# Kernel optimization log

Measured on AMD Instinct MI355X. Metric: run time of the kernel, lower is better.

The kernel has to match this reference:

```python
import jax, jax.numpy as jnp
import numpy as np

D_MODEL = 1024
N_HEADS = 16
N_KV_HEADS = 4
HEAD_DIM = D_MODEL // N_HEADS  # 64
N_REP = N_HEADS // N_KV_HEADS  # 4
THETA = 10000.0
LOGIT_CAP = 30.0
EPS = 1e-6
SCALE = HEAD_DIM ** -0.5


def rmsnorm(x, w):
    return x * jax.lax.rsqrt(jnp.mean(x * x, axis=-1, keepdims=True) + EPS) * w


def rope_tables(seq_len, dtype):
    inv_freq = 1.0 / (THETA ** (jnp.arange(0, HEAD_DIM, 2, dtype=jnp.float32) / HEAD_DIM))
    t = jnp.arange(seq_len, dtype=jnp.float32)
    freqs = jnp.outer(t, inv_freq)                      # [S, hd/2]
    emb = jnp.concatenate([freqs, freqs], axis=-1)      # [S, hd]
    return jnp.cos(emb).astype(dtype), jnp.sin(emb).astype(dtype)


def rotate_half(x):
    x1, x2 = jnp.split(x, 2, axis=-1)
    return jnp.concatenate([-x2, x1], axis=-1)


def apply_rope(x, cos, sin):
    # x: [B, H, S, hd]; cos/sin: [S, hd] broadcast over (B, H)
    return x * cos + rotate_half(x) * sin


def setup_inputs() -> dict:
    key = jax.random.key(0)
    ks = jax.random.split(key, 7)
    B, S = 4, 2048
    w = 0.02
    return {
        "x": jax.random.normal(ks[0], (B, S, D_MODEL), dtype=jnp.float32),
        "Wq": jax.random.normal(ks[1], (N_HEADS * HEAD_DIM, D_MODEL), dtype=jnp.float32) * w,
        "Wk": jax.random.normal(ks[2], (N_KV_HEADS * HEAD_DIM, D_MODEL), dtype=jnp.float32) * w,
        "Wv": jax.random.normal(ks[3], (N_KV_HEADS * HEAD_DIM, D_MODEL), dtype=jnp.float32) * w,
        "Wo": jax.random.normal(ks[4], (D_MODEL, N_HEADS * HEAD_DIM), dtype=jnp.float32) * w,
        "q_norm_w": jnp.ones((HEAD_DIM,), dtype=jnp.float32),
        "k_norm_w": jnp.ones((HEAD_DIM,), dtype=jnp.float32),
    }


def reference(x, Wq, Wk, Wv, Wo, q_norm_w, k_norm_w):
    B, S, _ = x.shape
    # projections (nn.Linear: y = x @ W^T)
    q = (x @ Wq.T).reshape(B, S, N_HEADS, HEAD_DIM).transpose(0, 2, 1, 3)      # [B,H,S,d]
    k = (x @ Wk.T).reshape(B, S, N_KV_HEADS, HEAD_DIM).transpose(0, 2, 1, 3)   # [B,Hkv,S,d]
    v = (x @ Wv.T).reshape(B, S, N_KV_HEADS, HEAD_DIM).transpose(0, 2, 1, 3)
    # QK-RMSNorm
    q = rmsnorm(q, q_norm_w)
    k = rmsnorm(k, k_norm_w)
    # RoPE
    cos, sin = rope_tables(S, x.dtype)
    q = apply_rope(q, cos, sin)
    k = apply_rope(k, cos, sin)
    # GQA expand (repeat_interleave over head dim)
    k_exp = jnp.repeat(k, N_REP, axis=1)  # [B,H,S,d]
    v_exp = jnp.repeat(v, N_REP, axis=1)
    # soft-capped attention (training path)
    scores = jnp.einsum('bhqd,bhkd->bhqk', q, k_exp) * SCALE
    scores = LOGIT_CAP * jnp.tanh(scores / LOGIT_CAP)
    causal = jnp.triu(jnp.ones((S, S), dtype=bool), k=1)  # kv_len - seq_len + 1 = 1
    scores = jnp.where(causal, -jnp.inf, scores)
    attn = jax.nn.softmax(scores, axis=-1)
    out = jnp.einsum('bhqk,bhkd->bhqd', attn, v_exp)
    out = out.transpose(0, 2, 1, 3).reshape(B, S, N_HEADS * HEAD_DIM)
    return out @ Wo.T
```

## Files before the change

kernel.cpp:

```cpp
#include <hip/hip_runtime.h>
#include <hip/hip_bf16.h>
#include <math.h>
#include <stdint.h>

#define D_MODEL 1024
#define NHEADS  16
#define NKV     4
#define HD      64
#define SEQ     2048
#define BATCH   4
#define MTOK    (BATCH*SEQ)
#define NQKV    (D_MODEL + 2*NKV*HD)
#define ASCALE  0.125f
#define CAP     30.0f

using f32x4  = __attribute__((ext_vector_type(4))) float;
using f32x2  = __attribute__((ext_vector_type(2))) float;
using bf16x8 = __attribute__((ext_vector_type(8))) short;
using u32x4  = __attribute__((ext_vector_type(4))) unsigned int;

__device__ __forceinline__ unsigned short f2bf(float f) {
  union { float f; unsigned u; } v; v.f = f;
  unsigned u = v.u + 0x7fffu + ((v.u >> 16) & 1u);
  return (unsigned short)(u >> 16);
}
__device__ __forceinline__ unsigned short f2bf_hup(float f) {
  union { float f; unsigned u; } v; v.f = f;
  return (unsigned short)((v.u + 0x8000u) >> 16);
}
__device__ __forceinline__ float fexp2(float x) {
  return __builtin_amdgcn_exp2f(x);
}
__device__ __forceinline__ void async_copy16(void* lds, const void* g) {
  __builtin_amdgcn_global_load_lds(
      (const __attribute__((address_space(1))) unsigned int*)(uintptr_t)g,
      (__attribute__((address_space(3))) unsigned int*)(uintptr_t)lds, 16, 0, 0);
}

__global__ __launch_bounds__(256) void cvt_all(
    const float* __restrict__ x, const float* __restrict__ wq,
    const float* __restrict__ wk, const float* __restrict__ wv,
    const float* __restrict__ wo,
    unsigned short* __restrict__ xb, unsigned short* __restrict__ wqkv,
    unsigned short* __restrict__ wob) {
  const long i = (long)(blockIdx.x * 256 + threadIdx.x) * 4;
  const float* src; unsigned short* dst; long off;
  if (i < 8388608L)      { src = x;  dst = xb;             off = i; }
  else if (i < 9437184L) { src = wq; dst = wqkv;           off = i - 8388608L; }
  else if (i < 9699328L) { src = wk; dst = wqkv + 1048576; off = i - 9437184L; }
  else if (i < 9961472L) { src = wv; dst = wqkv + 1310720; off = i - 9699328L; }
  else                   { src = wo; dst = wob;            off = i - 9961472L; }
  float4 v = *(const float4*)(src + off);
  ushort4 o; o.x = f2bf(v.x); o.y = f2bf(v.y); o.z = f2bf(v.z); o.w = f2bf(v.w);
  *(ushort4*)(dst + off) = o;
}

__global__ __launch_bounds__(256) void gemm_qkv(
    const unsigned short* __restrict__ A, const unsigned short* __restrict__ B,
    const float* __restrict__ qw, const float* __restrict__ kw,
    unsigned short* __restrict__ Qn, unsigned short* __restrict__ Kn,
    unsigned short* __restrict__ Vt) {
  __shared__ __align__(16) unsigned short As[2][128 * 32];
  __shared__ __align__(16) unsigned short Bs[2][128 * 32];
  const int t = threadIdx.x;
  const int w = t >> 6, l = t & 63;
  const int mb = blockIdx.x, nb = blockIdx.y;
  const int wm = w & 1, wn = w >> 1;
  const int quad = l >> 4, ln = l & 15;
  const int K = D_MODEL;
  f32x4 acc[4][4] = {};
  const unsigned short* Ag = A + (size_t)(mb * 128 + w * 32) * K;
  const unsigned short* Bg = B + (size_t)(nb * 128 + w * 32) * K;
  const int lrow = l >> 2, lcol = (l & 3) * 8;
  const int wo16 = w * 2048 + l * 16;

  async_copy16((char*)As[0] + wo16,        Ag + (size_t)lrow * K + lcol);
  async_copy16((char*)As[0] + wo16 + 1024, Ag + (size_t)(16 + lrow) * K + lcol);
  async_copy16((char*)Bs[0] + wo16,        Bg + (size_t)lrow * K + lcol);
  async_copy16((char*)Bs[0] + wo16 + 1024, Bg + (size_t)(16 + lrow) * K + lcol);

  int cur = 0;
  for (int kb = 0; kb < K; kb += 32) {
    __syncthreads();
    if (kb + 32 < K) {
      const int kn = kb + 32;
      async_copy16((char*)As[cur ^ 1] + wo16,        Ag + (size_t)lrow * K + kn + lcol);
      async_copy16((char*)As[cur ^ 1] + wo16 + 1024, Ag + (size_t)(16 + lrow) * K + kn + lcol);
      async_copy16((char*)Bs[cur ^ 1] + wo16,        Bg + (size_t)lrow * K + kn + lcol);
      async_copy16((char*)Bs[cur ^ 1] + wo16 + 1024, Bg + (size_t)(16 + lrow) * K + kn + lcol);
    }
    bf16x8 af[4], bfr[4];
#pragma unroll
    for (int mt = 0; mt < 4; ++mt)
      af[mt] = *(const bf16x8*)(As[cur] + (wm * 64 + mt * 16 + ln) * 32 + quad * 8);
#pragma unroll
    for (int nt = 0; nt < 4; ++nt)
      bfr[nt] = *(const bf16x8*)(Bs[cur] + (wn * 64 + nt * 16 + ln) * 32 + quad * 8);
#pragma unroll
    for (int mt = 0; mt < 4; ++mt)
#pragma unroll
      for (int nt = 0; nt < 4; ++nt)
        acc[mt][nt] = __builtin_amdgcn_mfma_f32_16x16x32_bf16(af[mt], bfr[nt], acc[mt][nt], 0, 0, 0);
    cur ^= 1;
  }

  const int hs = nb * 2 + wn;
  const int bB = mb >> 4;
  const int sBase = ((mb & 15) * 128) + wm * 64;

  if (hs < 20) {
    const float* wgt = (hs < 16) ? qw : kw;
    float wv_[4];
#pragma unroll
    for (int nt = 0; nt < 4; ++nt) wv_[nt] = wgt[nt * 16 + ln];
    const float f0 = __expf(-(float)ln * 0.2878231366f);
    const float f1 = f0 * 0.01f;
    unsigned short* dst = (hs < 16)
        ? Qn + (size_t)(bB * 16 + hs) * SEQ * 64
        : Kn + (size_t)(bB * 4 + (hs - 16)) * SEQ * 64;
#pragma unroll
    for (int mt = 0; mt < 4; ++mt) {
#pragma unroll
      for (int r = 0; r < 4; ++r) {
        const int sTok = sBase + mt * 16 + quad * 4 + r;
        float ss = 0.f;
#pragma unroll
        for (int nt = 0; nt < 4; ++nt) ss = fmaf(acc[mt][nt][r], acc[mt][nt][r], ss);
        ss += __shfl_xor(ss, 1, 64); ss += __shfl_xor(ss, 2, 64);
        ss += __shfl_xor(ss, 4, 64); ss += __shfl_xor(ss, 8, 64);
        const float inv = rsqrtf(ss * (1.0f / 64.0f) + 1e-6f);
        float xn[4];
#pragma unroll
        for (int nt = 0; nt < 4; ++nt) xn[nt] = acc[mt][nt][r] * inv * wv_[nt];
        float sn0, cs0, sn1, cs1;
        __sincosf((float)sTok * f0, &sn0, &cs0);
        __sincosf((float)sTok * f1, &sn1, &cs1);
        const float o0 = xn[0] * cs0 - xn[2] * sn0;
        const float o1 = xn[1] * cs1 - xn[3] * sn1;
        const float o2 = xn[2] * cs0 + xn[0] * sn0;
        const float o3 = xn[3] * cs1 + xn[1] * sn1;
        const size_t ro = (size_t)sTok * 64 + ln;
        dst[ro]      = f2bf(o0);
        dst[ro + 16] = f2bf(o1);
        dst[ro + 32] = f2bf(o2);
        dst[ro + 48] = f2bf(o3);
      }
    }
  } else {
    unsigned short* dst = Vt + (size_t)(bB * 4 + (hs - 20)) * 64 * SEQ;
#pragma unroll
    for (int mt = 0; mt < 4; ++mt)
#pragma unroll
      for (int nt = 0; nt < 4; ++nt)
#pragma unroll
        for (int r = 0; r < 4; ++r) {
          const int sTok = sBase + mt * 16 + quad * 4 + r;
          dst[(size_t)(nt * 16 + ln) * SEQ + sTok] = f2bf(acc[mt][nt][r]);
        }
  }
}

__global__ __launch_bounds__(256) void gemm_bt_f32(
    const unsigned short* __restrict__ A, const unsigned short* __restrict__ B,
    float* __restrict__ C, int M, int N, int K) {
  __shared__ __align__(16) unsigned short As[2][128 * 32];
  __shared__ __align__(16) unsigned short Bs[2][128 * 32];
  const int t = threadIdx.x;
  const int w = t >> 6, l = t & 63;
  const int mb = blockIdx.x, nb = blockIdx.y;
  const int wm = w & 1, wn = w >> 1;
  f32x4 acc[4][4] = {};
  const unsigned short* Ag = A + (size_t)(mb * 128 + w * 32) * K;
  const unsigned short* Bg = B + (size_t)(nb * 128 + w * 32) * K;
  const int lrow = l >> 2, lcol = (l & 3) * 8;
  const int wo16 = w * 2048 + l * 16;

  async_copy16((char*)As[0] + wo16,        Ag + (size_t)lrow * K + lcol);
  async_copy16((char*)As[0] + wo16 + 1024, Ag + (size_t)(16 + lrow) * K + lcol);
  async_copy16((char*)Bs[0] + wo16,        Bg + (size_t)lrow * K + lcol);
  async_copy16((char*)Bs[0] + wo16 + 1024, Bg + (size_t)(16 + lrow) * K + lcol);

  int cur = 0;
  for (int kb = 0; kb < K; kb += 32) {
    __syncthreads();
    if (kb + 32 < K) {
      const int kn = kb + 32;
      async_copy16((char*)As[cur ^ 1] + wo16,        Ag + (size_t)lrow * K + kn + lcol);
      async_copy16((char*)As[cur ^ 1] + wo16 + 1024, Ag + (size_t)(16 + lrow) * K + kn + lcol);
      async_copy16((char*)Bs[cur ^ 1] + wo16,        Bg + (size_t)lrow * K + kn + lcol);
      async_copy16((char*)Bs[cur ^ 1] + wo16 + 1024, Bg + (size_t)(16 + lrow) * K + kn + lcol);
    }
    bf16x8 af[4], bfr[4];
#pragma unroll
    for (int mt = 0; mt < 4; ++mt)
      af[mt] = *(const bf16x8*)(As[cur] + (wm * 64 + mt * 16 + (l & 15)) * 32 + (l >> 4) * 8);
#pragma unroll
    for (int nt = 0; nt < 4; ++nt)
      bfr[nt] = *(const bf16x8*)(Bs[cur] + (wn * 64 + nt * 16 + (l & 15)) * 32 + (l >> 4) * 8);
#pragma unroll
    for (int mt = 0; mt < 4; ++mt)
#pragma unroll
      for (int nt = 0; nt < 4; ++nt)
        acc[mt][nt] = __builtin_amdgcn_mfma_f32_16x16x32_bf16(af[mt], bfr[nt], acc[mt][nt], 0, 0, 0);
    cur ^= 1;
  }
  const int row0 = mb * 128 + wm * 64, col0 = nb * 128 + wn * 64;
#pragma unroll
  for (int mt = 0; mt < 4; ++mt)
#pragma unroll
    for (int nt = 0; nt < 4; ++nt)
#pragma unroll
      for (int r = 0; r < 4; ++r) {
        int row = row0 + mt * 16 + (l >> 4) * 4 + r;
        int col = col0 + nt * 16 + (l & 15);
        C[(size_t)row * N + col] = acc[mt][nt][r];
      }
}

__global__ __launch_bounds__(256, 4) void attn(
    const unsigned short* __restrict__ Qn, const unsigned short* __restrict__ Kn,
    const unsigned short* __restrict__ Vtg, unsigned short* __restrict__ O) {
  __shared__ __align__(16) unsigned short Ks[2][4096];
  __shared__ __align__(16) unsigned short Vs[2][4096];
  const int t = threadIdx.x, w = t >> 6, l = t & 63;
  const int quad = l >> 4, ln = l & 15;
  const int bid = blockIdx.x;
  const int qt = 15 - (bid >> 6);
  const int bh = bid & 63;
  const int h = bh & 15, b = bh >> 4;
  const int q0 = qt * 128;
  const int wq0 = q0 + w * 32;
  const unsigned short* Qh = Qn + ((size_t)(b * 16 + h)) * SEQ * 64;
  const unsigned short* Kg = Kn + ((size_t)(b * 4 + (h >> 2))) * SEQ * 64;
  const unsigned short* Vg = Vtg + ((size_t)(b * 4 + (h >> 2))) * 64 * SEQ;
  const int lrow = l >> 2;
  const int lswz = (((l & 3) ^ ((lrow >> 1) & 3)) * 8);
  const int qsw = (quad ^ ((ln >> 1) & 3)) << 4;

  bf16x8 aq[2][2];
#pragma unroll
  for (int mt = 0; mt < 2; ++mt)
#pragma unroll
    for (int ks = 0; ks < 2; ++ks)
      aq[mt][ks] = *(const bf16x8*)(Qh + (size_t)(wq0 + mt * 16 + ln) * 64 + ks * 32 + quad * 8);
  f32x4 o_acc[2][4] = {};
  f32x2 lp[2] = {};

  const float Cc = 0.18033688011112042f;
  const float B1 = -5.787037037e-6f;
  const float M2 = 11.541560327f;
  const int qr0 = wq0 + ln;

  const int jmax = 2 * qt + 2;

#pragma unroll
  for (int i = 0; i < 2; ++i) {
    int s = w * 2 + i;
    int snt = s >> 1, sks = s & 1;
    async_copy16((char*)Ks[0] + s * 1024,
                 Kg + (size_t)(snt * 16 + lrow) * 64 + sks * 32 + lswz);
    async_copy16((char*)Vs[0] + s * 1024,
                 Vg + (size_t)(snt * 16 + lrow) * SEQ + sks * 32 + lswz);
  }

  for (int jj = 0; jj < jmax; ++jj) {
    const int kv0 = jj * 64;
    const int cur = jj & 1;
    __syncthreads();
    if (jj + 1 < jmax) {
      const int kvn = kv0 + 64;
#pragma unroll
      for (int i = 0; i < 2; ++i) {
        int s = w * 2 + i;
        int snt = s >> 1, sks = s & 1;
        async_copy16((char*)Ks[cur ^ 1] + s * 1024,
                     Kg + (size_t)(kvn + snt * 16 + lrow) * 64 + sks * 32 + lswz);
        async_copy16((char*)Vs[cur ^ 1] + s * 1024,
                     Vg + (size_t)(snt * 16 + lrow) * SEQ + kvn + sks * 32 + lswz);
      }
    }
    if (kv0 > wq0 + 31) continue;

    f32x4 st[4][2] = {};
    __builtin_amdgcn_s_setprio(1);
#pragma unroll
    for (int nt = 0; nt < 4; ++nt)
#pragma unroll
      for (int ks = 0; ks < 2; ++ks) {
        bf16x8 bk = *(const bf16x8*)((char*)Ks[cur] + (nt * 2 + ks) * 1024 + ln * 64 + qsw);
        st[nt][0] = __builtin_amdgcn_mfma_f32_16x16x32_bf16(bk, aq[0][ks], st[nt][0], 0, 0, 0);
        st[nt][1] = __builtin_amdgcn_mfma_f32_16x16x32_bf16(bk, aq[1][ks], st[nt][1], 0, 0, 0);
      }
    __builtin_amdgcn_s_setprio(0);

    const bool needMask = (kv0 + 63 > wq0);
    bf16x8 ap[2][2];
#pragma unroll
    for (int mt = 0; mt < 2; ++mt) {
      const int qrow = qr0 + mt * 16;
      unsigned Wp[4][2];
#pragma unroll
      for (int nt = 0; nt < 4; ++nt)
#pragma unroll
        for (int rp = 0; rp < 2; ++rp) {
          f32x2 s = { st[nt][mt][rp * 2], st[nt][mt][rp * 2 + 1] };
          f32x2 s2 = s * s;
          f32x2 tt = s2 * B1 + 1.0f;
          f32x2 arg = (s * Cc) * tt - M2;
          float pr0 = fexp2(arg.x), pr1 = fexp2(arg.y);
          if (needMask) {
            const int kvb = kv0 + nt * 16 + quad * 4 + rp * 2;
            if (kvb > qrow)     pr0 = 0.0f;
            if (kvb + 1 > qrow) pr1 = 0.0f;
          }
          lp[mt] += (f32x2){pr0, pr1};
          unsigned wpk;
          asm("v_cvt_pk_bf16_f32 %0, %1, %2" : "=v"(wpk) : "v"(pr0), "v"(pr1));
          Wp[nt][rp] = wpk;
        }
#pragma unroll
      for (int ks = 0; ks < 2; ++ks) {
        unsigned a0 = Wp[2 * ks][0], b0 = Wp[2 * ks + 1][0];
        unsigned a1 = Wp[2 * ks][1], b1 = Wp[2 * ks + 1][1];
        asm("v_permlane32_swap_b32 %0, %1" : "+v"(a0), "+v"(b0));
        asm("v_permlane16_swap_b32 %0, %1" : "+v"(a0), "+v"(b0));
        asm("v_permlane32_swap_b32 %0, %1" : "+v"(a1), "+v"(b1));
        asm("v_permlane16_swap_b32 %0, %1" : "+v"(a1), "+v"(b1));
        union { u32x4 u; bf16x8 bv; } cc;
        cc.u = (u32x4){a0, a1, b0, b1};
        ap[mt][ks] = cc.bv;
      }
    }

    __builtin_amdgcn_s_setprio(1);
#pragma unroll
    for (int nt = 0; nt < 4; ++nt)
#pragma unroll
      for (int ks = 0; ks < 2; ++ks) {
        bf16x8 bv = *(const bf16x8*)((char*)Vs[cur] + (nt * 2 + ks) * 1024 + ln * 64 + qsw);
        o_acc[0][nt] = __builtin_amdgcn_mfma_f32_16x16x32_bf16(ap[0][ks], bv, o_acc[0][nt], 0, 0, 0);
        o_acc[1][nt] = __builtin_amdgcn_mfma_f32_16x16x32_bf16(ap[1][ks], bv, o_acc[1][nt], 0, 0, 0);
      }
    __builtin_amdgcn_s_setprio(0);
  }

  float invl[2][4];
#pragma unroll
  for (int mt = 0; mt < 2; ++mt) {
    float s = lp[mt].x + lp[mt].y;
    s += __shfl_xor(s, 16, 64);
    s += __shfl_xor(s, 32, 64);
#pragma unroll
    for (int r = 0; r < 4; ++r)
      invl[mt][r] = __builtin_amdgcn_rcpf(__shfl(s, quad * 4 + r, 64));
  }
#pragma unroll
  for (int mt = 0; mt < 2; ++mt)
#pragma unroll
    for (int nt = 0; nt < 4; ++nt)
#pragma unroll
      for (int r = 0; r < 4; ++r) {
        int qrow = wq0 + mt * 16 + quad * 4 + r;
        int col = h * 64 + nt * 16 + ln;
        O[((size_t)(b * SEQ + qrow)) * 1024 + col] = f2bf_hup(o_acc[mt][nt][r] * invl[mt][r]);
      }
}

extern "C" void kernel_launch(void* const* d_in, const int* in_sizes, int n_in,
                              void* d_out, int out_size, void* d_ws, size_t ws_size,
                              hipStream_t stream) {
  const float* x  = (const float*)d_in[0];
  const float* Wq = (const float*)d_in[1];
  const float* Wk = (const float*)d_in[2];
  const float* Wv = (const float*)d_in[3];
  const float* Wo = (const float*)d_in[4];
  const float* qw = (const float*)d_in[5];
  const float* kw = (const float*)d_in[6];
  float* out = (float*)d_out;

  char* ws = (char*)d_ws;
  unsigned short* xb   = (unsigned short*)(ws);
  unsigned short* wqkv = (unsigned short*)(ws + 16777216);
  unsigned short* wo   = (unsigned short*)(ws + 19922944);
  unsigned short* Qn   = (unsigned short*)(ws + 22020096);
  unsigned short* Kn   = (unsigned short*)(ws + 38797312);
  unsigned short* Vtg  = (unsigned short*)(ws + 42991616);
  unsigned short* Ob   = (unsigned short*)(ws + 47185920);

  cvt_all<<<10752, 256, 0, stream>>>(x, Wq, Wk, Wv, Wo, xb, wqkv, wo);
  gemm_qkv<<<dim3(MTOK / 128, NQKV / 128), 256, 0, stream>>>(xb, wqkv, qw, kw, Qn, Kn, Vtg);
  attn<<<1024, 256, 0, stream>>>(Qn, Kn, Vtg, Ob);
  gemm_bt_f32<<<dim3(MTOK / 128, 1024 / 128), 256, 0, stream>>>(Ob, wo, out, MTOK, 1024, 1024);
}
```

Baseline: 214.8 us.

## Enlarge projection GEMM tiles to 256x256 with 512-thread blocks

Both the fused QKV GEMM and the output projection GEMM now use 256x256 output tiles per block with 8 waves (2x4), each wave computing 128x64. This raises arithmetic intensity per LDS load and halves global reloads of A/B tiles. MFMA bursts are bracketed with s_setprio so that compute waves are favoured. The trade-off is fewer blocks (e.g. 32x6 and 32x4 grids on a 256-CU device), which risks underfilling the GPU, plus higher register pressure from 32 accumulators per lane.

```diff
diff --git a/kernel.cpp b/kernel.cpp
--- a/kernel.cpp
+++ b/kernel.cpp
@@ -55,58 +55,64 @@
   *(ushort4*)(dst + off) = o;
 }
 
-__global__ __launch_bounds__(256) void gemm_qkv(
+__global__ __launch_bounds__(512, 2) void gemm_qkv(
     const unsigned short* __restrict__ A, const unsigned short* __restrict__ B,
     const float* __restrict__ qw, const float* __restrict__ kw,
     unsigned short* __restrict__ Qn, unsigned short* __restrict__ Kn,
     unsigned short* __restrict__ Vt) {
-  __shared__ __align__(16) unsigned short As[2][128 * 32];
-  __shared__ __align__(16) unsigned short Bs[2][128 * 32];
+  __shared__ __align__(16) unsigned short LA[2][8192];
+  __shared__ __align__(16) unsigned short LB[2][8192];
   const int t = threadIdx.x;
   const int w = t >> 6, l = t & 63;
+  const int quad = l >> 4, ln = l & 15;
+  const int wm = w >> 2, wn = w & 3;
   const int mb = blockIdx.x, nb = blockIdx.y;
-  const int wm = w & 1, wn = w >> 1;
-  const int quad = l >> 4, ln = l & 15;
   const int K = D_MODEL;
-  f32x4 acc[4][4] = {};
-  const unsigned short* Ag = A + (size_t)(mb * 128 + w * 32) * K;
-  const unsigned short* Bg = B + (size_t)(nb * 128 + w * 32) * K;
-  const int lrow = l >> 2, lcol = (l & 3) * 8;
-  const int wo16 = w * 2048 + l * 16;
-
-  async_copy16((char*)As[0] + wo16,        Ag + (size_t)lrow * K + lcol);
-  async_copy16((char*)As[0] + wo16 + 1024, Ag + (size_t)(16 + lrow) * K + lcol);
-  async_copy16((char*)Bs[0] + wo16,        Bg + (size_t)lrow * K + lcol);
-  async_copy16((char*)Bs[0] + wo16 + 1024, Bg + (size_t)(16 + lrow) * K + lcol);
+  f32x4 acc[8][4] = {};
+  const unsigned short* Ag = A + (size_t)(mb * 256) * K;
+  const unsigned short* Bg = B + (size_t)(nb * 256) * K;
+  const int srow = t >> 2;
+  const int scol = (t & 3) * 8;
+  const int dst16 = t * 16;
+  const int abase = wm * 8192 + ln * 64 + quad * 16;
+  const int bbase = wn * 4096 + ln * 64 + quad * 16;
+
+  async_copy16((char*)LA[0] + dst16,        Ag + (size_t)srow * K + scol);
+  async_copy16((char*)LA[0] + dst16 + 8192, Ag + (size_t)(srow + 128) * K + scol);
+  async_copy16((char*)LB[0] + dst16,        Bg + (size_t)srow * K + scol);
+  async_copy16((char*)LB[0] + dst16 + 8192, Bg + (size_t)(srow + 128) * K + scol);
 
   int cur = 0;
   for (int kb = 0; kb < K; kb += 32) {
     __syncthreads();
     if (kb + 32 < K) {
       const int kn = kb + 32;
-      async_copy16((char*)As[cur ^ 1] + wo16,        Ag + (size_t)lrow * K + kn + lcol);
-      async_copy16((char*)As[cur ^ 1] + wo16 + 1024, Ag + (size_t)(16 + lrow) * K + kn + lcol);
-      async_copy16((char*)Bs[cur ^ 1] + wo16,        Bg + (size_t)lrow * K + kn + lcol);
-      async_copy16((char*)Bs[cur ^ 1] + wo16 + 1024, Bg + (size_t)(16 + lrow) * K + kn + lcol);
+      char* pa = (char*)LA[cur ^ 1]; char* pb = (char*)LB[cur ^ 1];
+      async_copy16(pa + dst16,        Ag + (size_t)srow * K + kn + scol);
+      async_copy16(pa + dst16 + 8192, Ag + (size_t)(srow + 128) * K + kn + scol);
+      async_copy16(pb + dst16,        Bg + (size_t)srow * K + kn + scol);
+      async_copy16(pb + dst16 + 8192, Bg + (size_t)(srow + 128) * K + kn + scol);
     }
-    bf16x8 af[4], bfr[4];
-#pragma unroll
-    for (int mt = 0; mt < 4; ++mt)
-      af[mt] = *(const bf16x8*)(As[cur] + (wm * 64 + mt * 16 + ln) * 32 + quad * 8);
-#pragma unroll
-    for (int nt = 0; nt < 4; ++nt)
-      bfr[nt] = *(const bf16x8*)(Bs[cur] + (wn * 64 + nt * 16 + ln) * 32 + quad * 8);
-#pragma unroll
-    for (int mt = 0; mt < 4; ++mt)
+    bf16x8 bf[4], af[8];
+#pragma unroll
+    for (int nt = 0; nt < 4; ++nt)
+      bf[nt] = *(const bf16x8*)((char*)LB[cur] + bbase + nt * 1024);
+#pragma unroll
+    for (int mt = 0; mt < 8; ++mt)
+      af[mt] = *(const bf16x8*)((char*)LA[cur] + abase + mt * 1024);
+    __builtin_amdgcn_s_setprio(1);
+#pragma unroll
+    for (int mt = 0; mt < 8; ++mt)
 #pragma unroll
       for (int nt = 0; nt < 4; ++nt)
-        acc[mt][nt] = __builtin_amdgcn_mfma_f32_16x16x32_bf16(af[mt], bfr[nt], acc[mt][nt], 0, 0, 0);
+        acc[mt][nt] = __builtin_amdgcn_mfma_f32_16x16x32_bf16(af[mt], bf[nt], acc[mt][nt], 0, 0, 0);
+    __builtin_amdgcn_s_setprio(0);
     cur ^= 1;
   }
 
-  const int hs = nb * 2 + wn;
-  const int bB = mb >> 4;
-  const int sBase = ((mb & 15) * 128) + wm * 64;
+  const int hs = nb * 4 + wn;
+  const int bB = mb >> 3;
+  const int sBase = ((mb & 7) * 256) + wm * 128;
 
   if (hs < 20) {
     const float* wgt = (hs < 16) ? qw : kw;
@@ -119,7 +125,7 @@
         ? Qn + (size_t)(bB * 16 + hs) * SEQ * 64
         : Kn + (size_t)(bB * 4 + (hs - 16)) * SEQ * 64;
 #pragma unroll
-    for (int mt = 0; mt < 4; ++mt) {
+    for (int mt = 0; mt < 8; ++mt) {
 #pragma unroll
       for (int r = 0; r < 4; ++r) {
         const int sTok = sBase + mt * 16 + quad * 4 + r;
@@ -149,7 +155,7 @@
   } else {
     unsigned short* dst = Vt + (size_t)(bB * 4 + (hs - 20)) * 64 * SEQ;
 #pragma unroll
-    for (int mt = 0; mt < 4; ++mt)
+    for (int mt = 0; mt < 8; ++mt)
 #pragma unroll
       for (int nt = 0; nt < 4; ++nt)
 #pragma unroll
@@ -160,59 +166,66 @@
   }
 }
 
-__global__ __launch_bounds__(256) void gemm_bt_f32(
+__global__ __launch_bounds__(512, 2) void gemm_bt_f32(
     const unsigned short* __restrict__ A, const unsigned short* __restrict__ B,
     float* __restrict__ C, int M, int N, int K) {
-  __shared__ __align__(16) unsigned short As[2][128 * 32];
-  __shared__ __align__(16) unsigned short Bs[2][128 * 32];
+  __shared__ __align__(16) unsigned short LA[2][8192];
+  __shared__ __align__(16) unsigned short LB[2][8192];
   const int t = threadIdx.x;
   const int w = t >> 6, l = t & 63;
+  const int quad = l >> 4, ln = l & 15;
+  const int wm = w >> 2, wn = w & 3;
   const int mb = blockIdx.x, nb = blockIdx.y;
-  const int wm = w & 1, wn = w >> 1;
-  f32x4 acc[4][4] = {};
-  const unsigned short* Ag = A + (size_t)(mb * 128 + w * 32) * K;
-  const unsigned short* Bg = B + (size_t)(nb * 128 + w * 32) * K;
-  const int lrow = l >> 2, lcol = (l & 3) * 8;
-  const int wo16 = w * 2048 + l * 16;
-
-  async_copy16((char*)As[0] + wo16,        Ag + (size_t)lrow * K + lcol);
-  async_copy16((char*)As[0] + wo16 + 1024, Ag + (size_t)(16 + lrow) * K + lcol);
-  async_copy16((char*)Bs[0] + wo16,        Bg + (size_t)lrow * K + lcol);
-  async_copy16((char*)Bs[0] + wo16 + 1024, Bg + (size_t)(16 + lrow) * K + lcol);
+  f32x4 acc[8][4] = {};
+  const unsigned short* Ag = A + (size_t)(mb * 256) * K;
+  const unsigned short* Bg = B + (size_t)(nb * 256) * K;
+  const int srow = t >> 2;
+  const int scol = (t & 3) * 8;
+  const int dst16 = t * 16;
+  const int abase = wm * 8192 + ln * 64 + quad * 16;
+  const int bbase = wn * 4096 + ln * 64 + quad * 16;
+
+  async_copy16((char*)LA[0] + dst16,        Ag + (size_t)srow * K + scol);
+  async_copy16((char*)LA[0] + dst16 + 8192, Ag + (size_t)(srow + 128) * K + scol);
+  async_copy16((char*)LB[0] + dst16,        Bg + (size_t)srow * K + scol);
+  async_copy16((char*)LB[0] + dst16 + 8192, Bg + (size_t)(srow + 128) * K + scol);
 
   int cur = 0;
   for (int kb = 0; kb < K; kb += 32) {
     __syncthreads();
     if (kb + 32 < K) {
       const int kn = kb + 32;
-      async_copy16((char*)As[cur ^ 1] + wo16,        Ag + (size_t)lrow * K + kn + lcol);
-      async_copy16((char*)As[cur ^ 1] + wo16 + 1024, Ag + (size_t)(16 + lrow) * K + kn + lcol);
-      async_copy16((char*)Bs[cur ^ 1] + wo16,        Bg + (size_t)lrow * K + kn + lcol);
-      async_copy16((char*)Bs[cur ^ 1] + wo16 + 1024, Bg + (size_t)(16 + lrow) * K + kn + lcol);
+      char* pa = (char*)LA[cur ^ 1]; char* pb = (char*)LB[cur ^ 1];
+      async_copy16(pa + dst16,        Ag + (size_t)srow * K + kn + scol);
+      async_copy16(pa + dst16 + 8192, Ag + (size_t)(srow + 128) * K + kn + scol);
+      async_copy16(pb + dst16,        Bg + (size_t)srow * K + kn + scol);
+      async_copy16(pb + dst16 + 8192, Bg + (size_t)(srow + 128) * K + kn + scol);
     }
-    bf16x8 af[4], bfr[4];
-#pragma unroll
-    for (int mt = 0; mt < 4; ++mt)
-      af[mt] = *(const bf16x8*)(As[cur] + (wm * 64 + mt * 16 + (l & 15)) * 32 + (l >> 4) * 8);
-#pragma unroll
-    for (int nt = 0; nt < 4; ++nt)
-      bfr[nt] = *(const bf16x8*)(Bs[cur] + (wn * 64 + nt * 16 + (l & 15)) * 32 + (l >> 4) * 8);
-#pragma unroll
-    for (int mt = 0; mt < 4; ++mt)
+    bf16x8 bf[4], af[8];
+#pragma unroll
+    for (int nt = 0; nt < 4; ++nt)
+      bf[nt] = *(const bf16x8*)((char*)LB[cur] + bbase + nt * 1024);
+#pragma unroll
+    for (int mt = 0; mt < 8; ++mt)
+      af[mt] = *(const bf16x8*)((char*)LA[cur] + abase + mt * 1024);
+    __builtin_amdgcn_s_setprio(1);
+#pragma unroll
+    for (int mt = 0; mt < 8; ++mt)
 #pragma unroll
       for (int nt = 0; nt < 4; ++nt)
-        acc[mt][nt] = __builtin_amdgcn_mfma_f32_16x16x32_bf16(af[mt], bfr[nt], acc[mt][nt], 0, 0, 0);
+        acc[mt][nt] = __builtin_amdgcn_mfma_f32_16x16x32_bf16(af[mt], bf[nt], acc[mt][nt], 0, 0, 0);
+    __builtin_amdgcn_s_setprio(0);
     cur ^= 1;
   }
-  const int row0 = mb * 128 + wm * 64, col0 = nb * 128 + wn * 64;
-#pragma unroll
-  for (int mt = 0; mt < 4; ++mt)
+  const int row0 = mb * 256 + wm * 128, col0 = nb * 256 + wn * 64;
+#pragma unroll
+  for (int mt = 0; mt < 8; ++mt)
 #pragma unroll
     for (int nt = 0; nt < 4; ++nt)
 #pragma unroll
       for (int r = 0; r < 4; ++r) {
-        int row = row0 + mt * 16 + (l >> 4) * 4 + r;
-        int col = col0 + nt * 16 + (l & 15);
+        int row = row0 + mt * 16 + quad * 4 + r;
+        int col = col0 + nt * 16 + ln;
         C[(size_t)row * N + col] = acc[mt][nt][r];
       }
 }
@@ -388,7 +401,7 @@
   unsigned short* Ob   = (unsigned short*)(ws + 47185920);
 
   cvt_all<<<10752, 256, 0, stream>>>(x, Wq, Wk, Wv, Wo, xb, wqkv, wo);
-  gemm_qkv<<<dim3(MTOK / 128, NQKV / 128), 256, 0, stream>>>(xb, wqkv, qw, kw, Qn, Kn, Vtg);
+  gemm_qkv<<<dim3(MTOK / 256, NQKV / 256), 512, 0, stream>>>(xb, wqkv, qw, kw, Qn, Kn, Vtg);
   attn<<<1024, 256, 0, stream>>>(Qn, Kn, Vtg, Ob);
-  gemm_bt_f32<<<dim3(MTOK / 128, 1024 / 128), 256, 0, stream>>>(Ob, wo, out, MTOK, 1024, 1024);
-}
+  gemm_bt_f32<<<dim3(MTOK / 256, 1024 / 256), 512, 0, stream>>>(Ob, wo, out, MTOK, 1024, 1024);
+}
```

New measurement: 229.0 us. +6.6%, slower.

## Fuse fp32-to-bf16 conversion of x into QKV GEMM A-tile loads

Applied to the files above, without the earlier changes.

The separate conversion pass over x is removed. The QKV GEMM now streams fp32 x tiles into a swizzled LDS buffer and converts them to bf16 with packed cvt instructions just before the MFMA. This saves a full read and write of the 32MB activation, at the cost of twice the LDS footprint and global traffic for the A tile, which is re-read once per N-block (12 times). It also folds one multiply out of the soft-cap polynomial in the attention inner loop by rescaling the coefficient.

```diff
diff --git a/kernel.cpp b/kernel.cpp
--- a/kernel.cpp
+++ b/kernel.cpp
@@ -37,30 +37,27 @@
       (__attribute__((address_space(3))) unsigned int*)(uintptr_t)lds, 16, 0, 0);
 }
 
-__global__ __launch_bounds__(256) void cvt_all(
-    const float* __restrict__ x, const float* __restrict__ wq,
-    const float* __restrict__ wk, const float* __restrict__ wv,
-    const float* __restrict__ wo,
-    unsigned short* __restrict__ xb, unsigned short* __restrict__ wqkv,
-    unsigned short* __restrict__ wob) {
+__global__ __launch_bounds__(256) void cvt_w(
+    const float* __restrict__ wq, const float* __restrict__ wk,
+    const float* __restrict__ wv, const float* __restrict__ wo,
+    unsigned short* __restrict__ wqkv, unsigned short* __restrict__ wob) {
   const long i = (long)(blockIdx.x * 256 + threadIdx.x) * 4;
   const float* src; unsigned short* dst; long off;
-  if (i < 8388608L)      { src = x;  dst = xb;             off = i; }
-  else if (i < 9437184L) { src = wq; dst = wqkv;           off = i - 8388608L; }
-  else if (i < 9699328L) { src = wk; dst = wqkv + 1048576; off = i - 9437184L; }
-  else if (i < 9961472L) { src = wv; dst = wqkv + 1310720; off = i - 9699328L; }
-  else                   { src = wo; dst = wob;            off = i - 9961472L; }
+  if (i < 1048576L)      { src = wq; dst = wqkv;           off = i; }
+  else if (i < 1310720L) { src = wk; dst = wqkv + 1048576; off = i - 1048576L; }
+  else if (i < 1572864L) { src = wv; dst = wqkv + 1310720; off = i - 1310720L; }
+  else                   { src = wo; dst = wob;            off = i - 1572864L; }
   float4 v = *(const float4*)(src + off);
   ushort4 o; o.x = f2bf(v.x); o.y = f2bf(v.y); o.z = f2bf(v.z); o.w = f2bf(v.w);
   *(ushort4*)(dst + off) = o;
 }
 
 __global__ __launch_bounds__(256) void gemm_qkv(
-    const unsigned short* __restrict__ A, const unsigned short* __restrict__ B,
+    const float* __restrict__ X, const unsigned short* __restrict__ B,
     const float* __restrict__ qw, const float* __restrict__ kw,
     unsigned short* __restrict__ Qn, unsigned short* __restrict__ Kn,
     unsigned short* __restrict__ Vt) {
-  __shared__ __align__(16) unsigned short As[2][128 * 32];
+  __shared__ __align__(16) float          Af[2][128 * 32];
   __shared__ __align__(16) unsigned short Bs[2][128 * 32];
   const int t = threadIdx.x;
   const int w = t >> 6, l = t & 63;
@@ -69,13 +66,22 @@
   const int quad = l >> 4, ln = l & 15;
   const int K = D_MODEL;
   f32x4 acc[4][4] = {};
-  const unsigned short* Ag = A + (size_t)(mb * 128 + w * 32) * K;
+  const float* Ag = X + (size_t)(mb * 128) * K;
   const unsigned short* Bg = B + (size_t)(nb * 128 + w * 32) * K;
   const int lrow = l >> 2, lcol = (l & 3) * 8;
   const int wo16 = w * 2048 + l * 16;
-
-  async_copy16((char*)As[0] + wo16,        Ag + (size_t)lrow * K + lcol);
-  async_copy16((char*)As[0] + wo16 + 1024, Ag + (size_t)(16 + lrow) * K + lcol);
+  int arow_[4], acol_[4];
+#pragma unroll
+  for (int i = 0; i < 4; ++i) {
+    const int s = t + i * 256;
+    arow_[i] = s >> 3;
+    acol_[i] = ((s & 7) ^ ((s >> 3) & 7)) * 4;
+  }
+
+#pragma unroll
+  for (int i = 0; i < 4; ++i)
+    async_copy16((char*)Af[0] + (t + i * 256) * 16,
+                 Ag + (size_t)arow_[i] * K + acol_[i]);
   async_copy16((char*)Bs[0] + wo16,        Bg + (size_t)lrow * K + lcol);
   async_copy16((char*)Bs[0] + wo16 + 1024, Bg + (size_t)(16 + lrow) * K + lcol);
 
@@ -84,15 +90,29 @@
     __syncthreads();
     if (kb + 32 < K) {
       const int kn = kb + 32;
-      async_copy16((char*)As[cur ^ 1] + wo16,        Ag + (size_t)lrow * K + kn + lcol);
-      async_copy16((char*)As[cur ^ 1] + wo16 + 1024, Ag + (size_t)(16 + lrow) * K + kn + lcol);
+#pragma unroll
+      for (int i = 0; i < 4; ++i)
+        async_copy16((char*)Af[cur ^ 1] + (t + i * 256) * 16,
+                     Ag + (size_t)arow_[i] * K + kn + acol_[i]);
       async_copy16((char*)Bs[cur ^ 1] + wo16,        Bg + (size_t)lrow * K + kn + lcol);
       async_copy16((char*)Bs[cur ^ 1] + wo16 + 1024, Bg + (size_t)(16 + lrow) * K + kn + lcol);
     }
     bf16x8 af[4], bfr[4];
 #pragma unroll
-    for (int mt = 0; mt < 4; ++mt)
-      af[mt] = *(const bf16x8*)(As[cur] + (wm * 64 + mt * 16 + ln) * 32 + quad * 8);
+    for (int mt = 0; mt < 4; ++mt) {
+      const int rr = wm * 64 + mt * 16 + ln;
+      const char* base = (const char*)Af[cur] + rr * 128;
+      const int sl0 = ((quad * 2)     ^ (rr & 7)) * 16;
+      const int sl1 = ((quad * 2 + 1) ^ (rr & 7)) * 16;
+      f32x4 v0 = *(const f32x4*)(base + sl0);
+      f32x4 v1 = *(const f32x4*)(base + sl1);
+      union { u32x4 u; bf16x8 b; } cv;
+      asm("v_cvt_pk_bf16_f32 %0, %1, %2" : "=v"(cv.u[0]) : "v"(v0.x), "v"(v0.y));
+      asm("v_cvt_pk_bf16_f32 %0, %1, %2" : "=v"(cv.u[1]) : "v"(v0.z), "v"(v0.w));
+      asm("v_cvt_pk_bf16_f32 %0, %1, %2" : "=v"(cv.u[2]) : "v"(v1.x), "v"(v1.y));
+      asm("v_cvt_pk_bf16_f32 %0, %1, %2" : "=v"(cv.u[3]) : "v"(v1.z), "v"(v1.w));
+      af[mt] = cv.b;
+    }
 #pragma unroll
     for (int nt = 0; nt < 4; ++nt)
       bfr[nt] = *(const bf16x8*)(Bs[cur] + (wn * 64 + nt * 16 + ln) * 32 + quad * 8);
@@ -246,9 +266,9 @@
   f32x4 o_acc[2][4] = {};
   f32x2 lp[2] = {};
 
-  const float Cc = 0.18033688011112042f;
-  const float B1 = -5.787037037e-6f;
-  const float M2 = 11.541560327f;
+  const float Cc  = 0.18033688011112042f;
+  const float B1c = -1.0436160e-6f;
+  const float M2  = 11.541560327f;
   const int qr0 = wq0 + ln;
 
   const int jmax = 2 * qt + 2;
@@ -305,8 +325,8 @@
         for (int rp = 0; rp < 2; ++rp) {
           f32x2 s = { st[nt][mt][rp * 2], st[nt][mt][rp * 2 + 1] };
           f32x2 s2 = s * s;
-          f32x2 tt = s2 * B1 + 1.0f;
-          f32x2 arg = (s * Cc) * tt - M2;
+          f32x2 tt = s2 * B1c + Cc;
+          f32x2 arg = s * tt - M2;
           float pr0 = fexp2(arg.x), pr1 = fexp2(arg.y);
           if (needMask) {
             const int kvb = kv0 + nt * 16 + quad * 4 + rp * 2;
@@ -379,7 +399,6 @@
   float* out = (float*)d_out;
 
   char* ws = (char*)d_ws;
-  unsigned short* xb   = (unsigned short*)(ws);
   unsigned short* wqkv = (unsigned short*)(ws + 16777216);
   unsigned short* wo   = (unsigned short*)(ws + 19922944);
   unsigned short* Qn   = (unsigned short*)(ws + 22020096);
@@ -387,8 +406,8 @@
   unsigned short* Vtg  = (unsigned short*)(ws + 42991616);
   unsigned short* Ob   = (unsigned short*)(ws + 47185920);
 
-  cvt_all<<<10752, 256, 0, stream>>>(x, Wq, Wk, Wv, Wo, xb, wqkv, wo);
-  gemm_qkv<<<dim3(MTOK / 128, NQKV / 128), 256, 0, stream>>>(xb, wqkv, qw, kw, Qn, Kn, Vtg);
+  cvt_w<<<2560, 256, 0, stream>>>(Wq, Wk, Wv, Wo, wqkv, wo);
+  gemm_qkv<<<dim3(MTOK / 128, NQKV / 128), 256, 0, stream>>>(x, wqkv, qw, kw, Qn, Kn, Vtg);
   attn<<<1024, 256, 0, stream>>>(Qn, Kn, Vtg, Ob);
   gemm_bt_f32<<<dim3(MTOK / 128, 1024 / 128), 256, 0, stream>>>(Ob, wo, out, MTOK, 1024, 1024);
 }
```

Result: slower. 223.0 us (+3.8%).
